# Performance work log

Hardware: AMD Instinct MI355X
Metric: run time of the kernel (lower is better)

Reference implementation:

```python
import jax, jax.numpy as jnp
import numpy as np

N = 4_000_000
G = 512          # input grid extent per axis
GP = G // 2      # parent (output) grid extent
SENT = jnp.iinfo(jnp.int32).max  # sort-stable sentinel for padded unique slots


def setup_inputs() -> dict:
    key = jax.random.key(0)
    k1, k2 = jax.random.split(key)
    coords = jax.random.randint(k1, (N, 4), 0, G, dtype=jnp.int32)
    coords = coords.at[:, 0].set(0)  # single batch
    feats = jax.random.normal(k2, (N, 1), dtype=jnp.float32)
    return {"coords": coords, "feats": feats}


def reference(coords, feats):
    # Sparse conv3d, kernel 2x2x2, stride 2, identity (8,1,8) weights ==
    # space-to-depth fold: out[parent, offset_id] = sum of inputs at that
    # offset inside the 2x2x2 block (sum handles duplicate coords like conv).
    b = coords[:, 0]
    xyz = coords[:, 1:]
    parent = xyz >> 1                     # [N,3] output voxel coords
    off = xyz & 1                         # [N,3] position within block
    offset_id = off[:, 0] * 4 + off[:, 1] * 2 + off[:, 2]  # lexicographic (dx,dy,dz)

    # Linearize parent voxel (batch-major) for dedup.
    key_lin = ((b * GP + parent[:, 0]) * GP + parent[:, 1]) * GP + parent[:, 2]

    # Fixed-size (jit-friendly) unique: sorted, padded at end with SENT.
    ukeys = jnp.unique(key_lin, size=N, fill_value=SENT)
    idx = jnp.searchsorted(ukeys, key_lin)  # row in output for each input point

    out_feats = jnp.zeros((N, 8), feats.dtype).at[idx, offset_id].add(feats[:, 0])

    # Decode output coords; mark padded rows with -1.
    kz = ukeys % GP
    ky = (ukeys // GP) % GP
    kx = (ukeys // (GP * GP)) % GP
    kb = ukeys // (GP * GP * GP)
    out_coords = jnp.stack([kb, kx, ky, kz], axis=1).astype(jnp.int32)
    valid = (ukeys != SENT)[:, None]
    out_coords = jnp.where(valid, out_coords, -1)
    return out_coords, out_feats
```

## Files before the change

kernel.cpp:

```cpp
#include <hip/hip_runtime.h>
#include <stdint.h>


static constexpr int      PTS_A  = 2048;
static constexpr int      PTS_B  = 4096;
static constexpr int      NB_A   = 64;
static constexpr int      SHARDS = 8;
static constexpr int      SEGS   = NB_A * SHARDS;
static constexpr uint32_t CAP_A  = 12288;
static constexpr int      BPS_B  = CAP_A / PTS_B;
static constexpr int      NB_B   = 256;
static constexpr int      NBKT   = NB_A * NB_B;
static constexpr uint32_t CAP_B  = 384;

__device__ __forceinline__ uint32_t make_pk(int4 c) {
    uint32_t key = ((((uint32_t)c.x << 8 | (uint32_t)(c.y >> 1)) << 8 |
                     (uint32_t)(c.z >> 1)) << 8) | (uint32_t)(c.w >> 1);
    uint32_t off = (uint32_t)(c.y & 1) * 4u + (uint32_t)(c.z & 1) * 2u + (uint32_t)(c.w & 1);
    return (key << 3) | off;
}

__device__ __forceinline__ uint32_t wave_incl_scan(uint32_t v, uint32_t lane) {
    #pragma unroll
    for (int d = 1; d < 64; d <<= 1) {
        uint32_t u = __shfl_up(v, d, 64);
        if (lane >= (uint32_t)d) v += u;
    }
    return v;
}

__global__ __launch_bounds__(256) void passA_kernel(const int4* __restrict__ coords,
                                                    const float* __restrict__ feats,
                                                    uint32_t* __restrict__ cursorA,
                                                    uint2* __restrict__ bufA, int n) {
    __shared__ uint32_t hist[NB_A], scx[NB_A], gbase[NB_A];
    __shared__ uint2 stage[PTS_A];
    int t = threadIdx.x, blk = blockIdx.x;
    int base = blk * PTS_A;
    if (t < NB_A) hist[t] = 0;
    __syncthreads();
    uint32_t pk[8]; float f[8]; uint16_t loc[8]; uint8_t bk[8];
    if (base + PTS_A <= n) {
        #pragma unroll
        for (int j = 0; j < 8; j++) {
            int i = base + j * 256 + t;
            pk[j] = make_pk(coords[i]);
            f[j] = feats[i];
            bk[j] = (uint8_t)(pk[j] >> 21);
            loc[j] = (uint16_t)atomicAdd(&hist[bk[j]], 1u);
        }
    } else {
        #pragma unroll
        for (int j = 0; j < 8; j++) {
            int i = base + j * 256 + t;
            if (i < n) {
                pk[j] = make_pk(coords[i]);
                f[j] = feats[i];
                bk[j] = (uint8_t)(pk[j] >> 21);
                loc[j] = (uint16_t)atomicAdd(&hist[bk[j]], 1u);
            } else pk[j] = 0xFFFFFFFFu;
        }
    }
    __syncthreads();
    if (t < NB_A) {
        uint32_t h = hist[t];
        uint32_t incl = wave_incl_scan(h, (uint32_t)t);
        uint32_t excl = incl - h;
        uint32_t shard = (uint32_t)t * SHARDS + (uint32_t)(blk & (SHARDS - 1));
        uint32_t old = atomicAdd(&cursorA[shard * 16], h);
        gbase[t] = shard * CAP_A + old;
        scx[t] = excl;
    }
    __syncthreads();
    #pragma unroll
    for (int j = 0; j < 8; j++)
        if (pk[j] != 0xFFFFFFFFu)
            stage[scx[bk[j]] + loc[j]] = make_uint2(pk[j], __float_as_uint(f[j]));
    int total = (base + PTS_A <= n) ? PTS_A : (n - base);
    __syncthreads();
    for (int s = t; s < total; s += 256) {
        uint2 p = stage[s];
        uint32_t b = p.x >> 21;
        bufA[gbase[b] + ((uint32_t)s - scx[b])] = p;
    }
}

__global__ __launch_bounds__(256) void passB_kernel(const uint2* __restrict__ bufA,
                                                    const uint32_t* __restrict__ cursorA,
                                                    uint32_t* __restrict__ cursorB,
                                                    uint32_t* __restrict__ bufBk,
                                                    float* __restrict__ bufBv) {
    __shared__ uint32_t hist[NB_B], scx[NB_B], gold[NB_B];
    __shared__ uint32_t wsum[4];
    __shared__ uint2 stage[PTS_B];
    int t = threadIdx.x, g = blockIdx.x;
    int sIdx = g / BPS_B, sub = g % BPS_B;
    uint32_t segBase = (uint32_t)sIdx * CAP_A;
    uint32_t segCnt = cursorA[sIdx * 16];
    if (segCnt > CAP_A) segCnt = CAP_A;
    int start = sub * PTS_B;
    int cnt = (int)segCnt - start;
    if (cnt > PTS_B) cnt = PTS_B;
    if (cnt < 0) cnt = 0;
    uint32_t aBase = (uint32_t)(sIdx >> 3) * NB_B;
    hist[t] = 0;
    __syncthreads();
    uint2 pr[16]; uint16_t loc[16]; uint8_t bk[16];
    #pragma unroll
    for (int j = 0; j < 16; j++) {
        int i = j * 256 + t;
        if (i < cnt) {
            pr[j] = bufA[segBase + start + i];
            bk[j] = (uint8_t)((pr[j].x >> 13) & 255u);
            loc[j] = (uint16_t)atomicAdd(&hist[bk[j]], 1u);
        }
    }
    __syncthreads();
    {
        uint32_t lane = (uint32_t)t & 63u, wave = (uint32_t)t >> 6;
        uint32_t h = hist[t];
        uint32_t incl = wave_incl_scan(h, lane);
        if (lane == 63u) wsum[wave] = incl;
        __syncthreads();
        uint32_t add = 0;
        #pragma unroll
        for (uint32_t w = 0; w < 4; w++) if (w < wave) add += wsum[w];
        incl += add;
        uint32_t excl = incl - h;
        gold[t] = atomicAdd(&cursorB[aBase + (uint32_t)t], h);
        scx[t] = excl;
    }
    __syncthreads();
    #pragma unroll
    for (int j = 0; j < 16; j++) {
        int i = j * 256 + t;
        if (i < cnt) stage[scx[bk[j]] + loc[j]] = pr[j];
    }
    __syncthreads();
    for (int s = t; s < cnt; s += 256) {
        uint2 p = stage[s];
        uint32_t b = (p.x >> 13) & 255u;
        uint32_t pos = gold[b] + ((uint32_t)s - scx[b]);
        if (pos < CAP_B) {
            uint32_t o = (aBase + b) * CAP_B + pos;
            bufBk[o] = p.x;
            bufBv[o] = __uint_as_float(p.y);
        }
    }
}

__global__ __launch_bounds__(256) void count_kernel(const uint32_t* __restrict__ bufBk,
                                                    const uint32_t* __restrict__ cursorB,
                                                    uint32_t* __restrict__ ucount,
                                                    uint32_t* __restrict__ bitmapG) {
    __shared__ uint32_t bm[32];
    int t = threadIdx.x, b = blockIdx.x;
    uint32_t cnt = cursorB[b]; if (cnt > CAP_B) cnt = CAP_B;
    if (t < 32) bm[t] = 0;
    __syncthreads();
    uint32_t base = (uint32_t)b * CAP_B;
    for (uint32_t i = t; i < cnt; i += 256) {
        uint32_t pk = bufBk[base + i];
        atomicOr(&bm[(pk >> 8) & 31u], 1u << ((pk >> 3) & 31u));
    }
    __syncthreads();
    if (t < 32) {
        uint32_t w = bm[t];
        bitmapG[(uint32_t)b * 32u + (uint32_t)t] = w;
        uint32_t s = (uint32_t)__popc(w);
        #pragma unroll
        for (int d = 1; d < 32; d <<= 1) s += __shfl_xor(s, d, 64);
        if (t == 0) ucount[b] = s;
    }
}

__global__ __launch_bounds__(1024) void scanU_kernel(const uint32_t* __restrict__ ucount,
                                                     uint32_t* __restrict__ baseRank,
                                                     uint32_t* __restrict__ totalOut) {
    __shared__ uint32_t s[1024];
    int t = threadIdx.x;
    uint32_t v[16]; uint32_t sum = 0;
    #pragma unroll
    for (int j = 0; j < 16; j++) { v[j] = ucount[t * 16 + j]; sum += v[j]; }
    s[t] = sum;
    __syncthreads();
    for (int d = 1; d < 1024; d <<= 1) {
        uint32_t x = (t >= d) ? s[t - d] : 0u;
        __syncthreads();
        s[t] += x;
        __syncthreads();
    }
    uint32_t run = s[t] - sum;
    #pragma unroll
    for (int j = 0; j < 16; j++) { baseRank[t * 16 + j] = run; run += v[j]; }
    if (t == 1023) *totalOut = s[1023];
}

__global__ __launch_bounds__(256) void fold_tail_kernel(const uint32_t* __restrict__ bufBk,
                                                        const float* __restrict__ bufBv,
                                                        const uint32_t* __restrict__ cursorB,
                                                        const uint32_t* __restrict__ bitmapG,
                                                        const uint32_t* __restrict__ baseRank,
                                                        const uint32_t* __restrict__ totalPtr,
                                                        float4* __restrict__ outCoords,
                                                        float4* __restrict__ outFeats2, int n) {
    __shared__ float acc[9216];
    __shared__ uint32_t bm[32], wp[32];
    __shared__ uint16_t keylist[1024];
    int t = threadIdx.x, b = blockIdx.x;
    uint32_t cnt = cursorB[b]; if (cnt > CAP_B) cnt = CAP_B;
    uint32_t base = (uint32_t)b * CAP_B;
    uint32_t k0 = 0u, k1 = 0u; float v0 = 0.f, v1 = 0.f;
    bool h0 = (uint32_t)t < cnt;
    bool h1 = (uint32_t)t + 256u < cnt;
    if (h0) { k0 = bufBk[base + (uint32_t)t];        v0 = bufBv[base + (uint32_t)t]; }
    if (h1) { k1 = bufBk[base + (uint32_t)t + 256u]; v1 = bufBv[base + (uint32_t)t + 256u]; }
    if (t < 32) bm[t] = bitmapG[(uint32_t)b * 32u + (uint32_t)t];
    __syncthreads();
    if (t < 32) {
        uint32_t s = (uint32_t)__popc(bm[t]);
        #pragma unroll
        for (int d = 1; d < 32; d <<= 1) {
            uint32_t u = __shfl_up(s, d, 64);
            if ((uint32_t)t >= (uint32_t)d) s += u;
        }
        wp[t] = s;
    }
    __syncthreads();
    for (int k = t; k < 1024; k += 256) {
        uint32_t w = (uint32_t)k >> 5, bit = (uint32_t)k & 31u, word = bm[w];
        if ((word >> bit) & 1u) {
            uint32_t lr = wp[w] - (uint32_t)__popc(word) + (uint32_t)__popc(word & ((1u << bit) - 1u));
            keylist[lr] = (uint16_t)k;
        }
    }
    __syncthreads();
    int ucnt = (int)wp[31];
    for (int u = t; u < ucnt; u += 256) {
        uint32_t k = keylist[u];
        #pragma unroll
        for (int j = 0; j < 8; j++) acc[k * 9u + (uint32_t)j] = 0.f;
    }
    __syncthreads();
    if (h0) atomicAdd(&acc[((k0 >> 3) & 1023u) * 9u + (k0 & 7u)], v0);
    if (h1) atomicAdd(&acc[((k1 >> 3) & 1023u) * 9u + (k1 & 7u)], v1);
    __syncthreads();
    uint32_t rbase = baseRank[b];
    for (int u = t; u < ucnt; u += 256) {
        uint32_t k = keylist[u];
        uint32_t rank = rbase + (uint32_t)u;
        uint32_t key = ((uint32_t)b << 10) | k;
        outCoords[rank] = make_float4((float)(key >> 24), (float)((key >> 16) & 255u),
                                      (float)((key >> 8) & 255u), (float)(key & 255u));
        float4 lo, hi;
        lo.x = acc[k * 9 + 0]; lo.y = acc[k * 9 + 1]; lo.z = acc[k * 9 + 2]; lo.w = acc[k * 9 + 3];
        hi.x = acc[k * 9 + 4]; hi.y = acc[k * 9 + 5]; hi.z = acc[k * 9 + 6]; hi.w = acc[k * 9 + 7];
        outFeats2[(size_t)rank * 2] = lo;
        outFeats2[(size_t)rank * 2 + 1] = hi;
    }
    float4 z4 = make_float4(0.f, 0.f, 0.f, 0.f);
    uint32_t U = *totalPtr;
    uint32_t rows = ((uint32_t)n > U) ? (uint32_t)n - U : 0u;
    uint32_t per = (rows + (uint32_t)gridDim.x - 1u) / (uint32_t)gridDim.x;
    uint32_t s0 = U + (uint32_t)b * per;
    uint32_t s1 = s0 + per; if (s1 > (uint32_t)n) s1 = (uint32_t)n;
    for (uint32_t i = s0 + (uint32_t)t; i < s1; i += 256u) {
        outCoords[i] = make_float4(-1.f, -1.f, -1.f, -1.f);
        outFeats2[(size_t)i * 2] = z4;
        outFeats2[(size_t)i * 2 + 1] = z4;
    }
}

static constexpr uint32_t NKEYS  = 1u << 24;
static constexpr uint32_t NWORDS = 1u << 19;
static constexpr int SCAN_BLOCKS = 512;

__global__ void zero_u4(uint4* __restrict__ p, int count) {
    int i = blockIdx.x * blockDim.x + threadIdx.x;
    int stride = gridDim.x * blockDim.x;
    uint4 z = {0u, 0u, 0u, 0u};
    for (; i < count; i += stride) p[i] = z;
}

__global__ void bytemark_kernel(const int4* __restrict__ coords, uint8_t* __restrict__ bytemap,
                                uint32_t* __restrict__ pkey, int n) {
    int i = blockIdx.x * blockDim.x + threadIdx.x;
    if (i >= n) return;
    uint32_t pk = make_pk(coords[i]);
    bytemap[pk >> 3] = 1;
    pkey[i] = pk;
}

__global__ void build_scan1_kernel(const uint4* __restrict__ bytemap4, uint4* __restrict__ bitmap4,
                                   uint32_t* __restrict__ blockSums) {
    __shared__ uint32_t red[256];
    int t = threadIdx.x;
    int base = blockIdx.x * 256 + t;
    uint4 wb;
    uint32_t* wordOut = (uint32_t*)&wb;
    uint32_t sum = 0;
    #pragma unroll
    for (int j = 0; j < 4; j++) {
        uint4 lo = bytemap4[base * 8 + j * 2];
        uint4 hi = bytemap4[base * 8 + j * 2 + 1];
        const uint32_t* cl = (const uint32_t*)&lo;
        const uint32_t* ch = (const uint32_t*)&hi;
        uint32_t bits = 0;
        #pragma unroll
        for (int k = 0; k < 4; k++)
            bits |= (((cl[k] & 0x01010101u) * 0x10204080u) >> 28) << (4 * k);
        #pragma unroll
        for (int k = 0; k < 4; k++)
            bits |= (((ch[k] & 0x01010101u) * 0x10204080u) >> 28) << (16 + 4 * k);
        wordOut[j] = bits;
        sum += (uint32_t)__popc(bits);
    }
    bitmap4[base] = wb;
    red[t] = sum;
    __syncthreads();
    for (int d = 128; d > 0; d >>= 1) {
        if (t < d) red[t] += red[t + d];
        __syncthreads();
    }
    if (t == 0) blockSums[blockIdx.x] = red[0];
}

__global__ void scan2_kernel(const uint32_t* __restrict__ blockSums, uint32_t* __restrict__ blockOffsets,
                             uint32_t* __restrict__ totalOut) {
    __shared__ uint32_t s[SCAN_BLOCKS];
    int t = threadIdx.x;
    uint32_t v = blockSums[t];
    s[t] = v;
    __syncthreads();
    for (int d = 1; d < SCAN_BLOCKS; d <<= 1) {
        uint32_t x = (t >= d) ? s[t - d] : 0u;
        __syncthreads();
        s[t] += x;
        __syncthreads();
    }
    blockOffsets[t] = s[t] - v;
    if (t == SCAN_BLOCKS - 1) *totalOut = s[t];
}

__global__ void scan3_kernel(const uint4* __restrict__ bitmap4, const uint32_t* __restrict__ blockOffsets,
                             uint4* __restrict__ wordPrefix4) {
    __shared__ uint32_t s[256];
    int t = threadIdx.x;
    int gi = blockIdx.x * 256 + t;
    uint4 w = bitmap4[gi];
    uint32_t p0 = __popc(w.x), p1 = __popc(w.y), p2 = __popc(w.z), p3 = __popc(w.w);
    uint32_t tot = p0 + p1 + p2 + p3;
    s[t] = tot;
    __syncthreads();
    for (int d = 1; d < 256; d <<= 1) {
        uint32_t x = (t >= d) ? s[t - d] : 0u;
        __syncthreads();
        s[t] += x;
        __syncthreads();
    }
    uint32_t excl = s[t] - tot + blockOffsets[blockIdx.x];
    uint4 wp;
    wp.x = excl; wp.y = wp.x + p0; wp.z = wp.y + p1; wp.w = wp.z + p2;
    wordPrefix4[gi] = wp;
}

__global__ void decode_kernel(const uint4* __restrict__ bitmap4, const uint4* __restrict__ wordPrefix4,
                              float4* __restrict__ outCoords) {
    int gi = blockIdx.x * blockDim.x + threadIdx.x;
    if (gi >= (int)(NWORDS / 4)) return;
    uint4 w = bitmap4[gi];
    uint4 wp = wordPrefix4[gi];
    uint32_t words[4] = {w.x, w.y, w.z, w.w};
    uint32_t prefs[4] = {wp.x, wp.y, wp.z, wp.w};
    #pragma unroll
    for (int j = 0; j < 4; j++) {
        uint32_t word = words[j];
        uint32_t rank = prefs[j];
        uint32_t baseKey = ((uint32_t)gi * 4u + (uint32_t)j) * 32u;
        while (word) {
            uint32_t bb = (uint32_t)__ffs(word) - 1u;
            word &= word - 1u;
            uint32_t key = baseKey + bb;
            outCoords[rank++] = make_float4((float)(key >> 24), (float)((key >> 16) & 255u),
                                            (float)((key >> 8) & 255u), (float)(key & 255u));
        }
    }
}

__global__ void tail_fill_kernel(float4* __restrict__ outCoords, float4* __restrict__ outFeats2,
                                 const uint32_t* __restrict__ totalPtr, int n) {
    int i = blockIdx.x * blockDim.x + threadIdx.x;
    if (i >= n) return;
    uint32_t U = *totalPtr;
    if ((uint32_t)i < U) return;
    outCoords[i] = make_float4(-1.f, -1.f, -1.f, -1.f);
    float4 z = make_float4(0.f, 0.f, 0.f, 0.f);
    outFeats2[(size_t)i * 2] = z;
    outFeats2[(size_t)i * 2 + 1] = z;
}

__global__ void scatter_pk_kernel(const uint32_t* __restrict__ pkey, const float* __restrict__ feats,
                                  const uint32_t* __restrict__ bitmap, const uint32_t* __restrict__ wordPrefix,
                                  float* __restrict__ outFeats, int n) {
    int i = blockIdx.x * blockDim.x + threadIdx.x;
    if (i >= n) return;
    uint32_t pk = pkey[i];
    uint32_t key = pk >> 3, off = pk & 7u;
    uint32_t w = key >> 5, bb = key & 31u;
    uint32_t idx = wordPrefix[w] + (uint32_t)__popc(bitmap[w] & ((1u << bb) - 1u));
    atomicAdd(outFeats + (size_t)idx * 8u + off, feats[i]);
}

extern "C" void kernel_launch(void* const* d_in, const int* in_sizes, int n_in,
                              void* d_out, int out_size, void* d_ws, size_t ws_size,
                              hipStream_t stream) {
    const int4* coords = (const int4*)d_in[0];
    const float* feats = (const float*)d_in[1];
    int n = in_sizes[0] / 4;

    float* out = (float*)d_out;
    float4* outCoords = (float4*)out;
    float* outFeats = out + (size_t)n * 4;
    float4* outFeats2 = (float4*)outFeats;

    uint8_t* ws = (uint8_t*)d_ws;
    int ptBlocks = (n + 255) / 256;

    uint32_t* cursorA  = (uint32_t*)ws;
    uint32_t* cursorB  = (uint32_t*)(ws + (32u << 10));
    uint32_t* ucountP  = (uint32_t*)(ws + (128u << 10));
    uint32_t* baseRank = (uint32_t*)(ws + (192u << 10));
    uint32_t* totalU   = (uint32_t*)(ws + (256u << 10));
    uint32_t* bitmapG  = (uint32_t*)(ws + (512u << 10));
    uint2*    bufA  = (uint2*)(ws + (4u << 20));
    uint32_t* bufBk = (uint32_t*)(ws + (4u << 20) + (size_t)SEGS * CAP_A * 8);
    float*    bufBv = (float*)(ws + (4u << 20) + (size_t)SEGS * CAP_A * 8
                               + (size_t)NBKT * CAP_B * 4);
    size_t need2 = (4u << 20) + (size_t)SEGS * CAP_A * 8 + (size_t)NBKT * CAP_B * 8;

    if (ws_size >= need2) {
        hipMemsetAsync(ws, 0, (96u << 10), stream);
        passA_kernel<<<(n + PTS_A - 1) / PTS_A, 256, 0, stream>>>(coords, feats, cursorA, bufA, n);
        passB_kernel<<<SEGS * BPS_B, 256, 0, stream>>>(bufA, cursorA, cursorB, bufBk, bufBv);
        count_kernel<<<NBKT, 256, 0, stream>>>(bufBk, cursorB, ucountP, bitmapG);
        scanU_kernel<<<1, 1024, 0, stream>>>(ucountP, baseRank, totalU);
        fold_tail_kernel<<<NBKT, 256, 0, stream>>>(bufBk, bufBv, cursorB, bitmapG, baseRank,
                                                   totalU, outCoords, outFeats2, n);
        return;
    }

    uint32_t* bitmap       = (uint32_t*)ws;
    uint32_t* wordPrefix   = (uint32_t*)(ws + (size_t)NWORDS * 4);
    uint32_t* blockSums    = (uint32_t*)(ws + (size_t)NWORDS * 8);
    uint32_t* blockOffsets = blockSums + SCAN_BLOCKS;
    uint32_t* totalPtr     = blockOffsets + SCAN_BLOCKS;
    uint8_t*  bytemap      = ws + (size_t)NWORDS * 8 + 8192;
    uint32_t* pkey         = (uint32_t*)(bytemap + NKEYS);

    zero_u4<<<2048, 256, 0, stream>>>((uint4*)outFeats, (int)(((size_t)n * 8) / 4));
    zero_u4<<<1024, 256, 0, stream>>>((uint4*)bytemap, (int)(NKEYS / 16));
    bytemark_kernel<<<ptBlocks, 256, 0, stream>>>(coords, bytemap, pkey, n);
    build_scan1_kernel<<<SCAN_BLOCKS, 256, 0, stream>>>((const uint4*)bytemap, (uint4*)bitmap, blockSums);
    scan2_kernel<<<1, SCAN_BLOCKS, 0, stream>>>(blockSums, blockOffsets, totalPtr);
    scan3_kernel<<<SCAN_BLOCKS, 256, 0, stream>>>((const uint4*)bitmap, blockOffsets, (uint4*)wordPrefix);
    decode_kernel<<<(int)(NWORDS / 4 + 255) / 256, 256, 0, stream>>>(
        (const uint4*)bitmap, (const uint4*)wordPrefix, outCoords);
    tail_fill_kernel<<<ptBlocks, 256, 0, stream>>>(outCoords, outFeats2, totalPtr, n);
    scatter_pk_kernel<<<ptBlocks, 256, 0, stream>>>(pkey, feats, bitmap, wordPrefix, outFeats, n);
}
```

Baseline: 354.0 us.

## Batch buckets per count block, wave-scan totals, compact fold accumulator

count_kernel now handles 16 buckets per block, locating each point's bucket with a binary search over per-bucket prefix counts, so the grid shrinks 16x and each block does more useful work. scanU replaces its barrier-heavy Hillis-Steele shared-memory scan with wave shuffle scans. fold_tail indexes its accumulator by local unique rank instead of raw key, cutting LDS from ~37KB to ~14KB for better occupancy, and removes one barrier phase by zeroing during load. This adds per-point rank computation and a serial prefix by thread 0.

```diff
diff --git a/kernel.cpp b/kernel.cpp
--- a/kernel.cpp
+++ b/kernel.cpp
@@ -12,6 +12,7 @@
 static constexpr int      NB_B   = 256;
 static constexpr int      NBKT   = NB_A * NB_B;
 static constexpr uint32_t CAP_B  = 384;
+static constexpr int      BKT_PER_CNT = 16;
 
 __device__ __forceinline__ uint32_t make_pk(int4 c) {
     uint32_t key = ((((uint32_t)c.x << 8 | (uint32_t)(c.y >> 1)) << 8 |
@@ -153,47 +154,72 @@
                                                     const uint32_t* __restrict__ cursorB,
                                                     uint32_t* __restrict__ ucount,
                                                     uint32_t* __restrict__ bitmapG) {
-    __shared__ uint32_t bm[32];
-    int t = threadIdx.x, b = blockIdx.x;
-    uint32_t cnt = cursorB[b]; if (cnt > CAP_B) cnt = CAP_B;
-    if (t < 32) bm[t] = 0;
-    __syncthreads();
-    uint32_t base = (uint32_t)b * CAP_B;
-    for (uint32_t i = t; i < cnt; i += 256) {
-        uint32_t pk = bufBk[base + i];
-        atomicOr(&bm[(pk >> 8) & 31u], 1u << ((pk >> 3) & 31u));
-    }
-    __syncthreads();
-    if (t < 32) {
-        uint32_t w = bm[t];
-        bitmapG[(uint32_t)b * 32u + (uint32_t)t] = w;
-        uint32_t s = (uint32_t)__popc(w);
-        #pragma unroll
-        for (int d = 1; d < 32; d <<= 1) s += __shfl_xor(s, d, 64);
-        if (t == 0) ucount[b] = s;
-    }
+    __shared__ uint32_t bm[BKT_PER_CNT * 32];
+    __shared__ uint32_t cshift[BKT_PER_CNT + 1];
+    __shared__ uint32_t ccnt[BKT_PER_CNT];
+    int t = threadIdx.x, g = blockIdx.x;
+    uint32_t b0 = (uint32_t)g * BKT_PER_CNT;
+    for (int i = t; i < BKT_PER_CNT * 32; i += 256) bm[i] = 0;
+    if (t < BKT_PER_CNT) {
+        uint32_t c = cursorB[b0 + (uint32_t)t]; if (c > CAP_B) c = CAP_B;
+        ccnt[t] = c;
+    }
+    __syncthreads();
+    if (t == 0) {
+        uint32_t r = 0;
+        #pragma unroll
+        for (int j = 0; j < BKT_PER_CNT; j++) { cshift[j] = r; r += ccnt[j]; }
+        cshift[BKT_PER_CNT] = r;
+    }
+    __syncthreads();
+    uint32_t Tp = cshift[BKT_PER_CNT];
+    for (uint32_t i = t; i < Tp; i += 256u) {
+        uint32_t bb = 0;
+        if (cshift[bb + 8] <= i) bb += 8;
+        if (cshift[bb + 4] <= i) bb += 4;
+        if (cshift[bb + 2] <= i) bb += 2;
+        if (cshift[bb + 1] <= i) bb += 1;
+        uint32_t pk = bufBk[(b0 + bb) * CAP_B + (i - cshift[bb])];
+        atomicOr(&bm[(bb << 5) + ((pk >> 8) & 31u)], 1u << ((pk >> 3) & 31u));
+    }
+    __syncthreads();
+    if (t < BKT_PER_CNT) {
+        uint32_t s = 0;
+        #pragma unroll
+        for (int w = 0; w < 32; w++) s += (uint32_t)__popc(bm[(t << 5) + w]);
+        ucount[b0 + (uint32_t)t] = s;
+    }
+    for (int i = t; i < BKT_PER_CNT * 32; i += 256)
+        bitmapG[(size_t)b0 * 32u + (uint32_t)i] = bm[i];
 }
 
 __global__ __launch_bounds__(1024) void scanU_kernel(const uint32_t* __restrict__ ucount,
                                                      uint32_t* __restrict__ baseRank,
                                                      uint32_t* __restrict__ totalOut) {
-    __shared__ uint32_t s[1024];
+    __shared__ uint32_t wsum[16];
     int t = threadIdx.x;
+    uint32_t lane = (uint32_t)t & 63u, wv = (uint32_t)t >> 6;
     uint32_t v[16]; uint32_t sum = 0;
     #pragma unroll
     for (int j = 0; j < 16; j++) { v[j] = ucount[t * 16 + j]; sum += v[j]; }
-    s[t] = sum;
-    __syncthreads();
-    for (int d = 1; d < 1024; d <<= 1) {
-        uint32_t x = (t >= d) ? s[t - d] : 0u;
-        __syncthreads();
-        s[t] += x;
-        __syncthreads();
-    }
-    uint32_t run = s[t] - sum;
+    uint32_t incl = wave_incl_scan(sum, lane);
+    if (lane == 63u) wsum[wv] = incl;
+    __syncthreads();
+    if (t < 16) {
+        uint32_t s = wsum[t];
+        #pragma unroll
+        for (int d = 1; d < 16; d <<= 1) {
+            uint32_t u = __shfl_up(s, d, 64);
+            if (t >= d) s += u;
+        }
+        wsum[t] = s;
+    }
+    __syncthreads();
+    uint32_t add = (wv > 0) ? wsum[wv - 1] : 0u;
+    uint32_t run = add + incl - sum;
     #pragma unroll
     for (int j = 0; j < 16; j++) { baseRank[t * 16 + j] = run; run += v[j]; }
-    if (t == 1023) *totalOut = s[1023];
+    if (t == 1023) *totalOut = add + incl;
 }
 
 __global__ __launch_bounds__(256) void fold_tail_kernel(const uint32_t* __restrict__ bufBk,
@@ -204,9 +230,9 @@
                                                         const uint32_t* __restrict__ totalPtr,
                                                         float4* __restrict__ outCoords,
                                                         float4* __restrict__ outFeats2, int n) {
-    __shared__ float acc[9216];
+    __shared__ float acc[384 * 9];
     __shared__ uint32_t bm[32], wp[32];
-    __shared__ uint16_t keylist[1024];
+    __shared__ uint16_t keylist[384];
     int t = threadIdx.x, b = blockIdx.x;
     uint32_t cnt = cursorB[b]; if (cnt > CAP_B) cnt = CAP_B;
     uint32_t base = (uint32_t)b * CAP_B;
@@ -216,6 +242,7 @@
     if (h0) { k0 = bufBk[base + (uint32_t)t];        v0 = bufBv[base + (uint32_t)t]; }
     if (h1) { k1 = bufBk[base + (uint32_t)t + 256u]; v1 = bufBv[base + (uint32_t)t + 256u]; }
     if (t < 32) bm[t] = bitmapG[(uint32_t)b * 32u + (uint32_t)t];
+    for (int i = t; i < 384 * 9; i += 256) acc[i] = 0.f;
     __syncthreads();
     if (t < 32) {
         uint32_t s = (uint32_t)__popc(bm[t]);
@@ -234,17 +261,18 @@
             keylist[lr] = (uint16_t)k;
         }
     }
+    if (h0) {
+        uint32_t kk = (k0 >> 3) & 1023u, w = kk >> 5, bit = kk & 31u;
+        uint32_t lr = wp[w] - (uint32_t)__popc(bm[w]) + (uint32_t)__popc(bm[w] & ((1u << bit) - 1u));
+        atomicAdd(&acc[lr * 9u + (k0 & 7u)], v0);
+    }
+    if (h1) {
+        uint32_t kk = (k1 >> 3) & 1023u, w = kk >> 5, bit = kk & 31u;
+        uint32_t lr = wp[w] - (uint32_t)__popc(bm[w]) + (uint32_t)__popc(bm[w] & ((1u << bit) - 1u));
+        atomicAdd(&acc[lr * 9u + (k1 & 7u)], v1);
+    }
     __syncthreads();
     int ucnt = (int)wp[31];
-    for (int u = t; u < ucnt; u += 256) {
-        uint32_t k = keylist[u];
-        #pragma unroll
-        for (int j = 0; j < 8; j++) acc[k * 9u + (uint32_t)j] = 0.f;
-    }
-    __syncthreads();
-    if (h0) atomicAdd(&acc[((k0 >> 3) & 1023u) * 9u + (k0 & 7u)], v0);
-    if (h1) atomicAdd(&acc[((k1 >> 3) & 1023u) * 9u + (k1 & 7u)], v1);
-    __syncthreads();
     uint32_t rbase = baseRank[b];
     for (int u = t; u < ucnt; u += 256) {
         uint32_t k = keylist[u];
@@ -253,8 +281,8 @@
         outCoords[rank] = make_float4((float)(key >> 24), (float)((key >> 16) & 255u),
                                       (float)((key >> 8) & 255u), (float)(key & 255u));
         float4 lo, hi;
-        lo.x = acc[k * 9 + 0]; lo.y = acc[k * 9 + 1]; lo.z = acc[k * 9 + 2]; lo.w = acc[k * 9 + 3];
-        hi.x = acc[k * 9 + 4]; hi.y = acc[k * 9 + 5]; hi.z = acc[k * 9 + 6]; hi.w = acc[k * 9 + 7];
+        lo.x = acc[u * 9 + 0]; lo.y = acc[u * 9 + 1]; lo.z = acc[u * 9 + 2]; lo.w = acc[u * 9 + 3];
+        hi.x = acc[u * 9 + 4]; hi.y = acc[u * 9 + 5]; hi.z = acc[u * 9 + 6]; hi.w = acc[u * 9 + 7];
         outFeats2[(size_t)rank * 2] = lo;
         outFeats2[(size_t)rank * 2 + 1] = hi;
     }
@@ -442,7 +470,7 @@
         hipMemsetAsync(ws, 0, (96u << 10), stream);
         passA_kernel<<<(n + PTS_A - 1) / PTS_A, 256, 0, stream>>>(coords, feats, cursorA, bufA, n);
         passB_kernel<<<SEGS * BPS_B, 256, 0, stream>>>(bufA, cursorA, cursorB, bufBk, bufBv);
-        count_kernel<<<NBKT, 256, 0, stream>>>(bufBk, cursorB, ucountP, bitmapG);
+        count_kernel<<<NBKT / BKT_PER_CNT, 256, 0, stream>>>(bufBk, cursorB, ucountP, bitmapG);
         scanU_kernel<<<1, 1024, 0, stream>>>(ucountP, baseRank, totalU);
         fold_tail_kernel<<<NBKT, 256, 0, stream>>>(bufBk, bufBv, cursorB, bitmapG, baseRank,
                                                    totalU, outCoords, outFeats2, n);
```

After: 341.5 us (median of 3 runs). 1.04x faster.
